# Performance work log

Hardware: AMD Instinct MI355X
Metric: run time of the kernel (lower is better)

The kernel has to match this reference:

```python
import jax, jax.numpy as jnp
import numpy as np

B, N, D = 8, 1024, 512
H, F = 8, 2048
Dh = D // H
EPS = 1e-5
NEG = -1.0e9


def _layernorm(x, g, b):
    mu = jnp.mean(x, axis=-1, keepdims=True)
    var = jnp.mean(jnp.square(x - mu), axis=-1, keepdims=True)
    return (x - mu) * jax.lax.rsqrt(var + EPS) * g + b


def setup_inputs() -> dict:
    key = jax.random.key(0)
    ks = jax.random.split(key, 8)
    s = 0.02  # weight init scale
    return {
        "x": jax.random.normal(ks[0], (B, N, D), jnp.float32),
        "adjacency_logits": jax.random.normal(ks[1], (N, N), jnp.float32),
        "candidate_edge_mask": jax.random.randint(ks[2], (N, N), 0, 2).astype(jnp.bool_),
        "Wq": jax.random.normal(ks[3], (D, D), jnp.float32) * s,
        "Wk": jax.random.normal(ks[4], (D, D), jnp.float32) * s,
        "Wv": jax.random.normal(ks[5], (D, D), jnp.float32) * s,
        "Wo": jax.random.normal(ks[6], (D, D), jnp.float32) * s,
        "W1": jax.random.normal(jax.random.fold_in(key, 10), (F, D), jnp.float32) * s,
        "b1": jnp.zeros((F,), jnp.float32),
        "W2": jax.random.normal(jax.random.fold_in(key, 11), (D, F), jnp.float32) * s,
        "b2": jnp.zeros((D,), jnp.float32),
        "g_ln1": jnp.ones((D,), jnp.float32),
        "beta_ln1": jnp.zeros((D,), jnp.float32),
        "g_ln2": jnp.ones((D,), jnp.float32),
        "beta_ln2": jnp.zeros((D,), jnp.float32),
    }


def reference(x, adjacency_logits, candidate_edge_mask, Wq, Wk, Wv, Wo,
              W1, b1, W2, b2, g_ln1, beta_ln1, g_ln2, beta_ln2):
    b, n, d = x.shape
    # projections: torch Linear is x @ W^T  -> [B,H,N,Dh]
    def proj(W):
        return jnp.einsum('bnd,ed->bne', x, W).reshape(b, n, H, Dh).transpose(0, 2, 1, 3)
    q, k, v = proj(Wq), proj(Wk), proj(Wv)
    scale = 1.0 / jnp.sqrt(jnp.float32(Dh))
    scores = jnp.einsum('bhqd,bhkd->bhqk', q, k) * scale
    scores = scores + adjacency_logits[None, None]
    mask = candidate_edge_mask[None, None]  # [1,1,N,N]
    scores = jnp.where(mask, scores, NEG)
    attn = jax.nn.softmax(scores, axis=-1)
    attn = jnp.where(mask, attn, 0.0)
    ctx = jnp.einsum('bhqk,bhkd->bhqd', attn, v)
    ctx = ctx.transpose(0, 2, 1, 3).reshape(b, n, d)
    attn_out = jnp.einsum('bnd,ed->bne', ctx, Wo)
    z = _layernorm(x + attn_out, g_ln1, beta_ln1)
    h = jax.nn.relu(jnp.einsum('bnd,fd->bnf', z, W1) + b1)
    z_ffn = jnp.einsum('bnf,df->bnd', h, W2) + b2
    out = _layernorm(z + z_ffn, g_ln2, beta_ln2)
    return out, attn.mean(axis=1)
```

## Files before the change

kernel.cpp:

```cpp
#include <hip/hip_runtime.h>
#include <math.h>
#include <stdint.h>


using bf16_t = __bf16;
typedef __attribute__((__ext_vector_type__(8))) __bf16 bf16x8;
typedef __attribute__((__ext_vector_type__(4))) __bf16 bf16x4;
typedef __attribute__((__ext_vector_type__(4))) float  f32x4;

#define DEVI __device__ __forceinline__

DEVI f32x4 mfma16(bf16x8 a, bf16x8 b, f32x4 c) {
  return __builtin_amdgcn_mfma_f32_16x16x32_bf16(a, b, c, 0, 0, 0);
}

DEVI void gload_lds16(const void* g, void* l) {
  __builtin_amdgcn_global_load_lds(
      (const __attribute__((address_space(1))) uint32_t*)g,
      (__attribute__((address_space(3))) uint32_t*)l, 16, 0, 0);
}

#define EPSC  (1e-5f)
#define QSCALE 0.18033688f

__global__ __launch_bounds__(256) void k_cvtall(const float* __restrict__ x,
                                                const float* __restrict__ wq,
                                                const float* __restrict__ wk,
                                                const float* __restrict__ wv,
                                                const float* __restrict__ wo,
                                                const float* __restrict__ w1,
                                                const float* __restrict__ w2,
                                                bf16_t* __restrict__ ox,
                                                bf16_t* __restrict__ owq,
                                                bf16_t* __restrict__ owk,
                                                bf16_t* __restrict__ owv,
                                                bf16_t* __restrict__ owo,
                                                bf16_t* __restrict__ ow1,
                                                bf16_t* __restrict__ ow2) {
  int blk = blockIdx.x;
  const float* src; bf16_t* dst; int base;
  if (blk < 4096)      { src = x;  dst = ox;  base = blk; }
  else {
    blk -= 4096;
    if      (blk < 256)  { src = wq; dst = owq; base = blk; }
    else if (blk < 512)  { src = wk; dst = owk; base = blk - 256; }
    else if (blk < 768)  { src = wv; dst = owv; base = blk - 512; }
    else if (blk < 1024) { src = wo; dst = owo; base = blk - 768; }
    else if (blk < 2048) { src = w1; dst = ow1; base = blk - 1024; }
    else                 { src = w2; dst = ow2; base = blk - 2048; }
  }
  int i = base * 256 + threadIdx.x;
  float4 v = ((const float4*)src)[i];
  bf16x4 o = { (__bf16)v.x, (__bf16)v.y, (__bf16)v.z, (__bf16)v.w };
  ((bf16x4*)dst)[i] = o;
}

__global__ __launch_bounds__(256) void k_prep(const float* __restrict__ adj,
                                              const int* __restrict__ msk,
                                              bf16_t* __restrict__ eadj) {
  int row  = blockIdx.x * 4 + (threadIdx.x >> 6);
  int lane = threadIdx.x & 63;
  for (int i = 0; i < 16; i++) {
    int c = lane + 64 * i;
    size_t idx = (size_t)row * 1024 + c;
    float a = adj[idx];
    bool valid = (msk[idx] != 0);
    eadj[idx] = valid ? (__bf16)__expf(a) : (__bf16)0.f;
  }
}

template<int EPI, int NSPLIT>
__global__ __launch_bounds__(256) void k_gemm(const bf16_t* __restrict__ A,
                                              const bf16_t* __restrict__ B,
                                              int K, int nbx,
                                              const float* __restrict__ bias,
                                              bf16_t* __restrict__ outb,
                                              float* __restrict__ outf,
                                              int out_ncols) {
  __shared__ bf16_t lA[2][4096];
  __shared__ bf16_t lB[2][4096];
  int bid = blockIdx.x;
  int bps = 64 * nbx;
  int split = bid / bps, r = bid - split * bps;
  int nb = r % nbx, mb = r / nbx;
  int KS = K / NSPLIT;
  const bf16_t* Ab = A + (size_t)split * KS;
  const bf16_t* Bb = B + (size_t)split * KS;
  int tid = threadIdx.x, wid = tid >> 6, lane = tid & 63;
  int l16 = lane & 15, g = lane >> 4;
  int wr = wid >> 1, wc = wid & 1;
  int rowbase = mb * 128, c0 = nb * 128;

  int dA0 = wid * 2048 + lane * 16;
  int rA0 = dA0 >> 6;
  int cbA = ((dA0 >> 4) & 3) ^ (rA0 & 3);
  const bf16_t* Asrc0 = Ab + (size_t)(rowbase + rA0) * K + cbA * 8;
  const bf16_t* Asrc1 = Ab + (size_t)(rowbase + rA0 + 16) * K + cbA * 8;
  const bf16_t* Bsrc0 = Bb + (size_t)(c0 + rA0) * K + cbA * 8;
  const bf16_t* Bsrc1 = Bb + (size_t)(c0 + rA0 + 16) * K + cbA * 8;

  f32x4 acc[4][4];
#pragma unroll
  for (int m = 0; m < 4; m++)
#pragma unroll
    for (int n = 0; n < 4; n++) acc[m][n] = (f32x4){0.f, 0.f, 0.f, 0.f};

  gload_lds16(Asrc0, (char*)&lA[0][0] + wid * 2048);
  gload_lds16(Asrc1, (char*)&lA[0][0] + wid * 2048 + 1024);
  gload_lds16(Bsrc0, (char*)&lB[0][0] + wid * 2048);
  gload_lds16(Bsrc1, (char*)&lB[0][0] + wid * 2048 + 1024);
  __syncthreads();

  for (int k0 = 0; k0 < KS; k0 += 32) {
    int buf = (k0 >> 5) & 1;
    if (k0 + 32 < KS) {
      gload_lds16(Asrc0 + k0 + 32, (char*)&lA[buf ^ 1][0] + wid * 2048);
      gload_lds16(Asrc1 + k0 + 32, (char*)&lA[buf ^ 1][0] + wid * 2048 + 1024);
      gload_lds16(Bsrc0 + k0 + 32, (char*)&lB[buf ^ 1][0] + wid * 2048);
      gload_lds16(Bsrc1 + k0 + 32, (char*)&lB[buf ^ 1][0] + wid * 2048 + 1024);
    }
    const char* cA = (const char*)&lA[buf][0];
    const char* cB = (const char*)&lB[buf][0];
    bf16x8 af[4], bq[4];
#pragma unroll
    for (int m = 0; m < 4; m++) {
      int row = wr * 64 + m * 16 + l16;
      af[m] = *(const bf16x8*)(cA + row * 64 + ((g ^ (row & 3)) << 4));
    }
#pragma unroll
    for (int n = 0; n < 4; n++) {
      int row = wc * 64 + n * 16 + l16;
      bq[n] = *(const bf16x8*)(cB + row * 64 + ((g ^ (row & 3)) << 4));
    }
#pragma unroll
    for (int m = 0; m < 4; m++)
#pragma unroll
      for (int n = 0; n < 4; n++) acc[m][n] = mfma16(af[m], bq[n], acc[m][n]);
    __syncthreads();
  }

  int which = c0 / out_ncols;
  int cloc0 = c0 - which * out_ncols;
  size_t obase = (size_t)which * 8192 * out_ncols +
                 (size_t)split * 8192 * out_ncols * (NSPLIT > 1 ? 1 : 0);
  float osc = (EPI == 0 && which == 0) ? QSCALE : 1.0f;
#pragma unroll
  for (int n = 0; n < 4; n++) {
    int col = cloc0 + wc * 64 + n * 16 + l16;
    float bv = (EPI >= 1 && bias && split == 0) ? bias[col] : 0.f;
#pragma unroll
    for (int m = 0; m < 4; m++)
#pragma unroll
      for (int j = 0; j < 4; j++) {
        int row = rowbase + wr * 64 + m * 16 + g * 4 + j;
        float v = acc[m][n][j] + bv;
        size_t idx = obase + (size_t)row * out_ncols + col;
        if (EPI == 1) outb[idx] = (__bf16)fmaxf(v, 0.f);
        else if (EPI == 0) outb[idx] = (__bf16)(v * osc);
        else outf[idx] = v;
      }
  }
}

__global__ __launch_bounds__(256) void k_resln(const float* __restrict__ gin,
                                               int nsplit,
                                               const float* __restrict__ residf,
                                               const bf16_t* __restrict__ residb,
                                               const float* __restrict__ gam,
                                               const float* __restrict__ bet,
                                               float* __restrict__ outf,
                                               bf16_t* __restrict__ outb) {
  const size_t GS = (size_t)8192 * 512;
  int row = blockIdx.x * 4 + (threadIdx.x >> 6);
  int lane = threadIdx.x & 63;
  const float* gp = gin + (size_t)row * 512;
  float4 a0 = ((const float4*)gp)[lane];
  float4 a1 = ((const float4*)gp)[lane + 64];
  for (int s = 1; s < nsplit; s++) {
    const float* gp2 = gp + s * GS;
    float4 r0 = ((const float4*)gp2)[lane];
    float4 r1 = ((const float4*)gp2)[lane + 64];
    a0.x += r0.x; a0.y += r0.y; a0.z += r0.z; a0.w += r0.w;
    a1.x += r1.x; a1.y += r1.y; a1.z += r1.z; a1.w += r1.w;
  }
  if (residf) {
    const float* rp = residf + (size_t)row * 512;
    float4 r0 = ((const float4*)rp)[lane];
    float4 r1 = ((const float4*)rp)[lane + 64];
    a0.x += r0.x; a0.y += r0.y; a0.z += r0.z; a0.w += r0.w;
    a1.x += r1.x; a1.y += r1.y; a1.z += r1.z; a1.w += r1.w;
  } else {
    const bf16_t* rp = residb + (size_t)row * 512;
    bf16x4 r0 = ((const bf16x4*)rp)[lane];
    bf16x4 r1 = ((const bf16x4*)rp)[lane + 64];
    a0.x += (float)r0[0]; a0.y += (float)r0[1]; a0.z += (float)r0[2]; a0.w += (float)r0[3];
    a1.x += (float)r1[0]; a1.y += (float)r1[1]; a1.z += (float)r1[2]; a1.w += (float)r1[3];
  }
  float s = a0.x + a0.y + a0.z + a0.w + a1.x + a1.y + a1.z + a1.w;
  for (int off = 1; off < 64; off <<= 1) s += __shfl_xor(s, off);
  float mu = s * (1.f / 512.f);
  float sq = (a0.x - mu) * (a0.x - mu) + (a0.y - mu) * (a0.y - mu) +
             (a0.z - mu) * (a0.z - mu) + (a0.w - mu) * (a0.w - mu) +
             (a1.x - mu) * (a1.x - mu) + (a1.y - mu) * (a1.y - mu) +
             (a1.z - mu) * (a1.z - mu) + (a1.w - mu) * (a1.w - mu);
  for (int off = 1; off < 64; off <<= 1) sq += __shfl_xor(sq, off);
  float rs = rsqrtf(sq * (1.f / 512.f) + EPSC);

  float4 g0 = ((const float4*)gam)[lane], g1v = ((const float4*)gam)[lane + 64];
  float4 b0 = ((const float4*)bet)[lane], b1v = ((const float4*)bet)[lane + 64];
  float4 o0, o1;
  o0.x = (a0.x - mu) * rs * g0.x + b0.x;  o0.y = (a0.y - mu) * rs * g0.y + b0.y;
  o0.z = (a0.z - mu) * rs * g0.z + b0.z;  o0.w = (a0.w - mu) * rs * g0.w + b0.w;
  o1.x = (a1.x - mu) * rs * g1v.x + b1v.x; o1.y = (a1.y - mu) * rs * g1v.y + b1v.y;
  o1.z = (a1.z - mu) * rs * g1v.z + b1v.z; o1.w = (a1.w - mu) * rs * g1v.w + b1v.w;
  if (outf) {
    float* op = outf + (size_t)row * 512;
    ((float4*)op)[lane] = o0;
    ((float4*)op)[lane + 64] = o1;
  }
  if (outb) {
    bf16_t* op = outb + (size_t)row * 512;
    bf16x4 q0 = { (__bf16)o0.x, (__bf16)o0.y, (__bf16)o0.z, (__bf16)o0.w };
    bf16x4 q1 = { (__bf16)o1.x, (__bf16)o1.y, (__bf16)o1.z, (__bf16)o1.w };
    ((bf16x4*)op)[lane] = q0;
    ((bf16x4*)op)[lane + 64] = q1;
  }
}

__global__ __launch_bounds__(256) void k_vtrans_knorm(const bf16_t* __restrict__ v,
                                                      bf16_t* __restrict__ vT,
                                                      const bf16_t* __restrict__ kk,
                                                      float* __restrict__ kmax) {
  __shared__ bf16_t t[64 * 66];
  __shared__ float red[4];
  int bid = blockIdx.x;
  int tid = threadIdx.x, wid = tid >> 6, lane = tid & 63;
  if (bid < 1024) {
    int nt = bid & 15, h = (bid >> 4) & 7, b = bid >> 7;
    for (int i = 0; i < 16; i++) {
      int n = wid * 16 + i;
      t[lane * 66 + n] = v[(size_t)(b * 1024 + nt * 64 + n) * 512 + h * 64 + lane];
    }
    __syncthreads();
    for (int i = 0; i < 16; i++) {
      int d = wid * 16 + i;
      vT[(size_t)((b * 8 + h) * 64 + d) * 1024 + nt * 64 + lane] = t[d * 66 + lane];
    }
  } else {
    int bh = bid - 1024;
    int b = bh >> 3, h = bh & 7;
    float mx = 0.f;
    for (int n = tid; n < 1024; n += 256) {
      const bf16_t* kp = kk + (size_t)(b * 1024 + n) * 512 + h * 64;
      float ss = 0.f;
#pragma unroll
      for (int vv = 0; vv < 8; vv++) {
        bf16x8 kv = *(const bf16x8*)(kp + vv * 8);
#pragma unroll
        for (int e = 0; e < 8; e++) { float f = (float)kv[e]; ss += f * f; }
      }
      mx = fmaxf(mx, ss);
    }
    for (int off = 1; off < 64; off <<= 1) mx = fmaxf(mx, __shfl_xor(mx, off));
    if (lane == 0) red[wid] = mx;
    __syncthreads();
    if (tid == 0) kmax[bh] = sqrtf(fmaxf(fmaxf(red[0], red[1]), fmaxf(red[2], red[3])));
  }
}

__global__ __launch_bounds__(512) void k_attn_ctx(const bf16_t* __restrict__ q,
                                                  const bf16_t* __restrict__ kk,
                                                  const bf16_t* __restrict__ vT,
                                                  const bf16_t* __restrict__ eadj,
                                                  const float* __restrict__ kmax,
                                                  bf16_t* __restrict__ ctx,
                                                  float* __restrict__ crl) {
  __shared__ bf16_t ldsK[2][4096];
  __shared__ bf16_t ldsV[2][4096];
  __shared__ bf16_t pt[8][16 * 68];
  int bid = blockIdx.x;
  int qt = bid >> 6, h = bid & 7, b = (bid >> 3) & 7;
  int tid = threadIdx.x, wid = tid >> 6, lane = tid & 63;
  int l16 = lane & 15, g = lane >> 4;
  int qg0 = qt * 128 + wid * 16;
  int kvbase = (b * 8 + h) * 64;

  int d0 = wid * 1024 + lane * 16;
  int row0 = d0 >> 7;
  int cb0 = ((d0 >> 4) & 7) ^ (row0 & 7);
  const bf16_t* ksrc = kk + (size_t)(b * 1024) * 512 + h * 64;
  const bf16_t* vsrc = vT + (size_t)kvbase * 1024;

  auto stage = [&](int buf, int kc0) {
    gload_lds16(ksrc + (size_t)(kc0 + row0) * 512 + cb0 * 8, &ldsK[buf][wid * 512]);
    gload_lds16(vsrc + (size_t)row0 * 1024 + kc0 + cb0 * 8, &ldsV[buf][wid * 512]);
  };

  const bf16_t* qp = q + (size_t)(b * 1024 + qg0 + l16) * 512 + h * 64 + 8 * g;
  bf16x8 aq0 = *(const bf16x8*)qp;
  bf16x8 aq1 = *(const bf16x8*)(qp + 32);

  float kmaxv = kmax[b * 8 + h];
  float ssq = 0.f;
#pragma unroll
  for (int e = 0; e < 8; e++) {
    float f0 = (float)aq0[e], f1 = (float)aq1[e];
    ssq += f0 * f0 + f1 * f1;
  }
  ssq += __shfl_xor(ssq, 16);
  ssq += __shfl_xor(ssq, 32);
  float Cn = sqrtf(ssq) * kmaxv;
  float Cj[4];
#pragma unroll
  for (int j = 0; j < 4; j++) Cj[j] = __shfl(Cn, g * 4 + j);

  f32x4 cacc[4];
#pragma unroll
  for (int d = 0; d < 4; d++) cacc[d] = (f32x4){0.f, 0.f, 0.f, 0.f};
  float ls[4] = {0.f, 0.f, 0.f, 0.f};
  bf16_t* myp = pt[wid];
  int rph = l16 & 7;
  const bf16_t* erow = eadj + (size_t)(qg0 + g * 4) * 1024 + l16;

  bf16_t eaA[4][4], eaB[4][4];
  stage(0, 0);
#pragma unroll
  for (int cg = 0; cg < 4; cg++)
#pragma unroll
    for (int j = 0; j < 4; j++) eaA[cg][j] = erow[(size_t)j * 1024 + cg * 16];
  __syncthreads();

  auto tile = [&](int kt, int buf, bf16_t (&eaC)[4][4], bf16_t (&eaN)[4][4]) {
    int kc0 = kt * 64;
    int ktn = (kt + 1 < 16) ? kt + 1 : 15;
    stage(buf ^ 1, ktn * 64);
#pragma unroll
    for (int cg = 0; cg < 4; cg++)
#pragma unroll
      for (int j = 0; j < 4; j++)
        eaN[cg][j] = erow[(size_t)j * 1024 + ktn * 64 + cg * 16];

    const char* curK = (const char*)ldsK[buf];
    const char* curV = (const char*)ldsV[buf];

#pragma unroll
    for (int cg = 0; cg < 4; cg++) {
      const char* krow = curK + ((cg * 16 + l16) << 7);
      bf16x8 k0 = *(const bf16x8*)(krow + ((g ^ rph) << 4));
      bf16x8 k1 = *(const bf16x8*)(krow + (((g + 4) ^ rph) << 4));
      f32x4 s = (f32x4){0.f, 0.f, 0.f, 0.f};
      __builtin_amdgcn_s_setprio(1);
      s = mfma16(aq0, k0, s);
      s = mfma16(aq1, k1, s);
      __builtin_amdgcn_s_setprio(0);
#pragma unroll
      for (int j = 0; j < 4; j++) {
        float p = (float)eaC[cg][j] * exp2f(s[j] - Cj[j]);
        ls[j] += p;
        myp[(g * 4 + j) * 68 + cg * 16 + l16] = (__bf16)p;
      }
    }
#pragma unroll
    for (int half = 0; half < 2; half++) {
      bf16x8 pa = *(const bf16x8*)(myp + l16 * 68 + half * 32 + 8 * g);
      __builtin_amdgcn_s_setprio(1);
#pragma unroll
      for (int dg = 0; dg < 4; dg++) {
        const char* vrow = curV + ((dg * 16 + l16) << 7);
        bf16x8 vv = *(const bf16x8*)(vrow + (((g + half * 4) ^ rph) << 4));
        cacc[dg] = mfma16(pa, vv, cacc[dg]);
      }
      __builtin_amdgcn_s_setprio(0);
    }
    __syncthreads();
  };

  for (int k2 = 0; k2 < 8; k2++) {
    tile(2 * k2,     0, eaA, eaB);
    tile(2 * k2 + 1, 1, eaB, eaA);
  }

#pragma unroll
  for (int j = 0; j < 4; j++)
    for (int off = 1; off < 16; off <<= 1) ls[j] += __shfl_xor(ls[j], off);
  float rc[4];
#pragma unroll
  for (int j = 0; j < 4; j++) rc[j] = (ls[j] > 0.f) ? (1.f / ls[j]) : 0.f;

#pragma unroll
  for (int dg = 0; dg < 4; dg++)
#pragma unroll
    for (int j = 0; j < 4; j++) {
      int row = qg0 + g * 4 + j;
      ctx[(size_t)(b * 1024 + row) * 512 + h * 64 + dg * 16 + l16] =
          (__bf16)(cacc[dg][j] * rc[j]);
    }
  if (l16 == 0) {
#pragma unroll
    for (int j = 0; j < 4; j++) {
      int li = (b * 8 + h) * 1024 + qg0 + g * 4 + j;
      crl[li] = (ls[j] > 0.f) ? (Cj[j] + __log2f(ls[j])) : 1.0e30f;
    }
  }
}

__global__ __launch_bounds__(256, 4) void k_attn_mean(const bf16_t* __restrict__ q,
                                                      const bf16_t* __restrict__ kk,
                                                      const bf16_t* __restrict__ eadj,
                                                      const float* __restrict__ crl,
                                                      float* __restrict__ mout) {
  __shared__ bf16_t lds[4][2][2048];
  int bid = blockIdx.x;
  int kq = bid & 7, qt = (bid >> 3) & 15, b = bid >> 7;
  int tid = threadIdx.x, wid = tid >> 6, lane = tid & 63;
  int l16 = lane & 15, g = lane >> 4;
  int qg0 = qt * 64 + wid * 16;
  int kbase = kq * 128;
  int rl = lane >> 3;
  int cb = (lane & 7) ^ rl;
  const bf16_t* ksrc = kk + (size_t)(b * 1024 + kbase) * 512;

  auto stage = [&](int t) {
    int h = t >> 2, c = t & 3;
    char* dst = (char*)&lds[wid][t & 1][0];
    const bf16_t* sp = ksrc + (size_t)(c * 32 + rl) * 512 + h * 64 + cb * 8;
#pragma unroll
    for (int i = 0; i < 4; i++)
      gload_lds16(sp + (size_t)i * 8 * 512, dst + i * 1024);
  };

  f32x4 macc[8];
#pragma unroll
  for (int kg = 0; kg < 8; kg++) macc[kg] = (f32x4){0.f, 0.f, 0.f, 0.f};

  stage(0);

  for (int h = 0; h < 8; h++) {
    const bf16_t* qp = q + (size_t)(b * 1024 + qg0 + l16) * 512 + h * 64 + 8 * g;
    bf16x8 aq0 = *(const bf16x8*)qp;
    bf16x8 aq1 = *(const bf16x8*)(qp + 32);
    f32x4 CR = *(const f32x4*)(crl + (b * 8 + h) * 1024 + qg0 + g * 4);
#pragma unroll
    for (int c = 0; c < 4; c++) {
      int t = h * 4 + c;
      __builtin_amdgcn_sched_barrier(0);
      if (t < 31) {
        stage(t + 1);
        __builtin_amdgcn_sched_barrier(0);
        asm volatile("s_waitcnt vmcnt(4)" ::: "memory");
      } else {
        asm volatile("s_waitcnt vmcnt(0)" ::: "memory");
      }
      __builtin_amdgcn_sched_barrier(0);
      const char* cK = (const char*)&lds[wid][t & 1][0];
#pragma unroll
      for (int cg = 0; cg < 2; cg++) {
        const char* krow = cK + ((cg * 16 + l16) << 7);
        bf16x8 k0 = *(const bf16x8*)(krow + ((g ^ (l16 & 7)) << 4));
        bf16x8 k1 = *(const bf16x8*)(krow + (((g + 4) ^ (l16 & 7)) << 4));
        f32x4 s = (f32x4){0.f, 0.f, 0.f, 0.f};
        __builtin_amdgcn_s_setprio(1);
        s = mfma16(aq0, k0, s);
        s = mfma16(aq1, k1, s);
        __builtin_amdgcn_s_setprio(0);
        int kg = c * 2 + cg;
#pragma unroll
        for (int j = 0; j < 4; j++)
          macc[kg][j] += exp2f(s[j] - CR[j]);
      }
    }
  }

#pragma unroll
  for (int kg = 0; kg < 8; kg++)
#pragma unroll
    for (int j = 0; j < 4; j++) {
      size_t off = (size_t)(qg0 + g * 4 + j) * 1024 + kbase + kg * 16 + l16;
      mout[(size_t)b * 1048576 + off] = macc[kg][j] * (float)eadj[off] * 0.125f;
    }
}

extern "C" void kernel_launch(void* const* d_in, const int* in_sizes, int n_in,
                              void* d_out, int out_size, void* d_ws, size_t ws_size,
                              hipStream_t stream) {
  (void)in_sizes; (void)n_in; (void)out_size; (void)ws_size;
  const float* x   = (const float*)d_in[0];
  const float* adj = (const float*)d_in[1];
  const int*   msk = (const int*)d_in[2];
  const float* Wq  = (const float*)d_in[3];
  const float* Wk  = (const float*)d_in[4];
  const float* Wv  = (const float*)d_in[5];
  const float* Wo  = (const float*)d_in[6];
  const float* W1  = (const float*)d_in[7];
  const float* b1  = (const float*)d_in[8];
  const float* W2  = (const float*)d_in[9];
  const float* b2  = (const float*)d_in[10];
  const float* g1  = (const float*)d_in[11];
  const float* be1 = (const float*)d_in[12];
  const float* g2  = (const float*)d_in[13];
  const float* be2 = (const float*)d_in[14];

  float* out  = (float*)d_out;
  float* mout = out + (size_t)8 * 1024 * 512;

  char* ws = (char*)d_ws;
  const size_t MB = 1024 * 1024;
  bf16_t* wqb = (bf16_t*)(ws);
  bf16_t* wkb = (bf16_t*)(ws + 512 * 1024);
  bf16_t* wvb = (bf16_t*)(ws + 1 * MB);
  bf16_t* wob = (bf16_t*)(ws + 3 * MB / 2);
  bf16_t* w1b = (bf16_t*)(ws + 2 * MB);
  bf16_t* w2b = (bf16_t*)(ws + 4 * MB);
  float*  crl  = (float*)(ws + 6 * MB + 256 * 1024);
  float*  kmax = (float*)(ws + 6 * MB + 768 * 1024);
  bf16_t* xb   = (bf16_t*)(ws + 8 * MB);
  bf16_t* ctx  = xb;
  bf16_t* zb   = xb;
  bf16_t* qb   = (bf16_t*)(ws + 16 * MB);
  bf16_t* kb   = (bf16_t*)(ws + 24 * MB);
  bf16_t* vb   = (bf16_t*)(ws + 32 * MB);
  bf16_t* vT   = (bf16_t*)(ws + 40 * MB);
  float*  gout1 = (float*)(ws + 16 * MB);
  bf16_t* hb    = (bf16_t*)(ws + 16 * MB);
  float*  gout2 = (float*)(ws + 44 * MB);
  bf16_t* eadj  = (bf16_t*)(ws + 72 * MB);

  k_cvtall<<<7168, 256, 0, stream>>>(x, Wq, Wk, Wv, Wo, W1, W2,
                                     xb, wqb, wkb, wvb, wob, w1b, w2b);

  k_prep<<<256, 256, 0, stream>>>(adj, msk, eadj);

  k_gemm<0, 1><<<64 * 12, 256, 0, stream>>>(xb, wqb, 512, 12, nullptr, qb, nullptr, 512);
  k_vtrans_knorm<<<1088, 256, 0, stream>>>(vb, vT, kb, kmax);

  k_attn_ctx<<<512, 512, 0, stream>>>(qb, kb, vT, eadj, kmax, ctx, crl);
  k_attn_mean<<<1024, 256, 0, stream>>>(qb, kb, eadj, crl, mout);

  k_gemm<2, 2><<<2 * 64 * 4, 256, 0, stream>>>(ctx, wob, 512, 4, nullptr, nullptr, gout1, 512);
  k_resln<<<2048, 256, 0, stream>>>(gout1, 2, x, nullptr, g1, be1, nullptr, zb);
  k_gemm<1, 1><<<64 * 16, 256, 0, stream>>>(zb, w1b, 512, 16, b1, hb, nullptr, 2048);
  k_gemm<2, 2><<<2 * 64 * 4, 256, 0, stream>>>(hb, w2b, 2048, 4, b2, nullptr, gout2, 512);
  k_resln<<<2048, 256, 0, stream>>>(gout2, 2, nullptr, zb, g2, be2, out, nullptr);
}
```

Baseline: 231.3 us.

## Triple-buffer attention K/V pipeline, permute eadj layout, fold prep into convert

Moves the exp(adjacency)/mask prep into the conversion kernel as extra blocks, dropping one launch. The prep now writes a permuted layout, so each lane reads its four adjacency weights as one bf16x4 vector instead of sixteen scalar loads. The attention-context kernel goes from double to triple buffering of K/V tiles, with explicit vmcnt waits and raw s_barrier replacing __syncthreads. The row max offset is folded into the MFMA accumulator init to save a subtract per element. The cost is more LDS per block, which may lower occupancy, and hand-tuned waitcnt counts that must match the number of loads in flight.

```diff
diff --git a/kernel.cpp b/kernel.cpp
--- a/kernel.cpp
+++ b/kernel.cpp
@@ -30,14 +30,30 @@
                                                 const float* __restrict__ wo,
                                                 const float* __restrict__ w1,
                                                 const float* __restrict__ w2,
+                                                const float* __restrict__ adj,
+                                                const int* __restrict__ msk,
                                                 bf16_t* __restrict__ ox,
                                                 bf16_t* __restrict__ owq,
                                                 bf16_t* __restrict__ owk,
                                                 bf16_t* __restrict__ owv,
                                                 bf16_t* __restrict__ owo,
                                                 bf16_t* __restrict__ ow1,
-                                                bf16_t* __restrict__ ow2) {
+                                                bf16_t* __restrict__ ow2,
+                                                bf16_t* __restrict__ eadjP) {
   int blk = blockIdx.x;
+  if (blk >= 7168) {
+    int row  = (blk - 7168) * 4 + (threadIdx.x >> 6);
+    int lane = threadIdx.x & 63;
+    for (int i = 0; i < 16; i++) {
+      int c = lane + 64 * i;
+      size_t idx = (size_t)row * 1024 + c;
+      float a = adj[idx];
+      bool valid = (msk[idx] != 0);
+      int pos = (c & ~63) + ((c & 15) << 2) + ((c >> 4) & 3);
+      eadjP[(size_t)row * 1024 + pos] = valid ? (__bf16)__expf(a) : (__bf16)0.f;
+    }
+    return;
+  }
   const float* src; bf16_t* dst; int base;
   if (blk < 4096)      { src = x;  dst = ox;  base = blk; }
   else {
@@ -53,20 +69,6 @@
   float4 v = ((const float4*)src)[i];
   bf16x4 o = { (__bf16)v.x, (__bf16)v.y, (__bf16)v.z, (__bf16)v.w };
   ((bf16x4*)dst)[i] = o;
-}
-
-__global__ __launch_bounds__(256) void k_prep(const float* __restrict__ adj,
-                                              const int* __restrict__ msk,
-                                              bf16_t* __restrict__ eadj) {
-  int row  = blockIdx.x * 4 + (threadIdx.x >> 6);
-  int lane = threadIdx.x & 63;
-  for (int i = 0; i < 16; i++) {
-    int c = lane + 64 * i;
-    size_t idx = (size_t)row * 1024 + c;
-    float a = adj[idx];
-    bool valid = (msk[idx] != 0);
-    eadj[idx] = valid ? (__bf16)__expf(a) : (__bf16)0.f;
-  }
 }
 
 template<int EPI, int NSPLIT>
@@ -271,12 +273,12 @@
 __global__ __launch_bounds__(512) void k_attn_ctx(const bf16_t* __restrict__ q,
                                                   const bf16_t* __restrict__ kk,
                                                   const bf16_t* __restrict__ vT,
-                                                  const bf16_t* __restrict__ eadj,
+                                                  const bf16_t* __restrict__ eadjP,
                                                   const float* __restrict__ kmax,
                                                   bf16_t* __restrict__ ctx,
                                                   float* __restrict__ crl) {
-  __shared__ bf16_t ldsK[2][4096];
-  __shared__ bf16_t ldsV[2][4096];
+  __shared__ bf16_t ldsK[3][4096];
+  __shared__ bf16_t ldsV[3][4096];
   __shared__ bf16_t pt[8][16 * 68];
   int bid = blockIdx.x;
   int qt = bid >> 6, h = bid & 7, b = (bid >> 3) & 7;
@@ -310,9 +312,9 @@
   ssq += __shfl_xor(ssq, 16);
   ssq += __shfl_xor(ssq, 32);
   float Cn = sqrtf(ssq) * kmaxv;
-  float Cj[4];
-#pragma unroll
-  for (int j = 0; j < 4; j++) Cj[j] = __shfl(Cn, g * 4 + j);
+  f32x4 negC;
+#pragma unroll
+  for (int j = 0; j < 4; j++) negC[j] = -__shfl(Cn, g * 4 + j);
 
   f32x4 cacc[4];
 #pragma unroll
@@ -320,42 +322,30 @@
   float ls[4] = {0.f, 0.f, 0.f, 0.f};
   bf16_t* myp = pt[wid];
   int rph = l16 & 7;
-  const bf16_t* erow = eadj + (size_t)(qg0 + g * 4) * 1024 + l16;
-
-  bf16_t eaA[4][4], eaB[4][4];
-  stage(0, 0);
-#pragma unroll
-  for (int cg = 0; cg < 4; cg++)
-#pragma unroll
-    for (int j = 0; j < 4; j++) eaA[cg][j] = erow[(size_t)j * 1024 + cg * 16];
-  __syncthreads();
-
-  auto tile = [&](int kt, int buf, bf16_t (&eaC)[4][4], bf16_t (&eaN)[4][4]) {
-    int kc0 = kt * 64;
-    int ktn = (kt + 1 < 16) ? kt + 1 : 15;
-    stage(buf ^ 1, ktn * 64);
-#pragma unroll
-    for (int cg = 0; cg < 4; cg++)
-#pragma unroll
-      for (int j = 0; j < 4; j++)
-        eaN[cg][j] = erow[(size_t)j * 1024 + ktn * 64 + cg * 16];
-
+  const bf16_t* erowP = eadjP + (size_t)(qg0 + g * 4) * 1024 + l16 * 4;
+
+  bf16x4 ea0[4], ea1[4];
+  auto loadEA = [&](bf16x4 (&d)[4], int kc0) {
+#pragma unroll
+    for (int j = 0; j < 4; j++)
+      d[j] = *(const bf16x4*)(erowP + (size_t)j * 1024 + kc0);
+  };
+
+  auto computeTile = [&](int buf, const bf16x4 (&eaC)[4]) {
     const char* curK = (const char*)ldsK[buf];
     const char* curV = (const char*)ldsV[buf];
-
 #pragma unroll
     for (int cg = 0; cg < 4; cg++) {
       const char* krow = curK + ((cg * 16 + l16) << 7);
       bf16x8 k0 = *(const bf16x8*)(krow + ((g ^ rph) << 4));
       bf16x8 k1 = *(const bf16x8*)(krow + (((g + 4) ^ rph) << 4));
-      f32x4 s = (f32x4){0.f, 0.f, 0.f, 0.f};
       __builtin_amdgcn_s_setprio(1);
-      s = mfma16(aq0, k0, s);
+      f32x4 s = mfma16(aq0, k0, negC);
       s = mfma16(aq1, k1, s);
       __builtin_amdgcn_s_setprio(0);
 #pragma unroll
       for (int j = 0; j < 4; j++) {
-        float p = (float)eaC[cg][j] * exp2f(s[j] - Cj[j]);
+        float p = (float)eaC[j][cg] * exp2f(s[j]);
         ls[j] += p;
         myp[(g * 4 + j) * 68 + cg * 16 + l16] = (__bf16)p;
       }
@@ -372,12 +362,37 @@
       }
       __builtin_amdgcn_s_setprio(0);
     }
-    __syncthreads();
   };
 
-  for (int k2 = 0; k2 < 8; k2++) {
-    tile(2 * k2,     0, eaA, eaB);
-    tile(2 * k2 + 1, 1, eaB, eaA);
+  stage(0, 0);
+  stage(1, 64);
+  loadEA(ea0, 0);
+  __builtin_amdgcn_sched_barrier(0);
+  asm volatile("s_waitcnt vmcnt(6) lgkmcnt(0)" ::: "memory");
+  __builtin_amdgcn_sched_barrier(0);
+  __builtin_amdgcn_s_barrier();
+  __builtin_amdgcn_sched_barrier(0);
+
+#pragma unroll
+  for (int kt = 0; kt < 16; ++kt) {
+    const int buf = kt % 3;
+    if (kt + 2 < 16) stage((kt + 2) % 3, (kt + 2) * 64);
+    if (kt + 1 < 16) {
+      if ((kt & 1) == 0) loadEA(ea1, (kt + 1) * 64);
+      else               loadEA(ea0, (kt + 1) * 64);
+    }
+    if ((kt & 1) == 0) computeTile(buf, ea0);
+    else               computeTile(buf, ea1);
+    if (kt < 15) {
+      __builtin_amdgcn_sched_barrier(0);
+      if (kt < 14)
+        asm volatile("s_waitcnt vmcnt(6) lgkmcnt(0)" ::: "memory");
+      else
+        asm volatile("s_waitcnt vmcnt(4) lgkmcnt(0)" ::: "memory");
+      __builtin_amdgcn_sched_barrier(0);
+      __builtin_amdgcn_s_barrier();
+      __builtin_amdgcn_sched_barrier(0);
+    }
   }
 
 #pragma unroll
@@ -399,14 +414,14 @@
 #pragma unroll
     for (int j = 0; j < 4; j++) {
       int li = (b * 8 + h) * 1024 + qg0 + g * 4 + j;
-      crl[li] = (ls[j] > 0.f) ? (Cj[j] + __log2f(ls[j])) : 1.0e30f;
+      crl[li] = (ls[j] > 0.f) ? (-negC[j] + __log2f(ls[j])) : 1.0e30f;
     }
   }
 }
 
 __global__ __launch_bounds__(256, 4) void k_attn_mean(const bf16_t* __restrict__ q,
                                                       const bf16_t* __restrict__ kk,
-                                                      const bf16_t* __restrict__ eadj,
+                                                      const bf16_t* __restrict__ eadjP,
                                                       const float* __restrict__ crl,
                                                       float* __restrict__ mout) {
   __shared__ bf16_t lds[4][2][2048];
@@ -440,6 +455,7 @@
     bf16x8 aq0 = *(const bf16x8*)qp;
     bf16x8 aq1 = *(const bf16x8*)(qp + 32);
     f32x4 CR = *(const f32x4*)(crl + (b * 8 + h) * 1024 + qg0 + g * 4);
+    f32x4 negCR = (f32x4){-CR[0], -CR[1], -CR[2], -CR[3]};
 #pragma unroll
     for (int c = 0; c < 4; c++) {
       int t = h * 4 + c;
@@ -458,15 +474,14 @@
         const char* krow = cK + ((cg * 16 + l16) << 7);
         bf16x8 k0 = *(const bf16x8*)(krow + ((g ^ (l16 & 7)) << 4));
         bf16x8 k1 = *(const bf16x8*)(krow + (((g + 4) ^ (l16 & 7)) << 4));
-        f32x4 s = (f32x4){0.f, 0.f, 0.f, 0.f};
         __builtin_amdgcn_s_setprio(1);
-        s = mfma16(aq0, k0, s);
+        f32x4 s = mfma16(aq0, k0, negCR);
         s = mfma16(aq1, k1, s);
         __builtin_amdgcn_s_setprio(0);
         int kg = c * 2 + cg;
 #pragma unroll
         for (int j = 0; j < 4; j++)
-          macc[kg][j] += exp2f(s[j] - CR[j]);
+          macc[kg][j] += exp2f(s[j]);
       }
     }
   }
@@ -475,8 +490,10 @@
   for (int kg = 0; kg < 8; kg++)
 #pragma unroll
     for (int j = 0; j < 4; j++) {
-      size_t off = (size_t)(qg0 + g * 4 + j) * 1024 + kbase + kg * 16 + l16;
-      mout[(size_t)b * 1048576 + off] = macc[kg][j] * (float)eadj[off] * 0.125f;
+      size_t row = qg0 + g * 4 + j;
+      size_t off = row * 1024 + kbase + kg * 16 + l16;
+      size_t poff = row * 1024 + 64 * (kq * 2 + (kg >> 2)) + l16 * 4 + (kg & 3);
+      mout[(size_t)b * 1048576 + off] = macc[kg][j] * (float)eadjP[poff] * 0.125f;
     }
 }
 
@@ -523,18 +540,16 @@
   float*  gout1 = (float*)(ws + 16 * MB);
   bf16_t* hb    = (bf16_t*)(ws + 16 * MB);
   float*  gout2 = (float*)(ws + 44 * MB);
-  bf16_t* eadj  = (bf16_t*)(ws + 72 * MB);
-
-  k_cvtall<<<7168, 256, 0, stream>>>(x, Wq, Wk, Wv, Wo, W1, W2,
-                                     xb, wqb, wkb, wvb, wob, w1b, w2b);
-
-  k_prep<<<256, 256, 0, stream>>>(adj, msk, eadj);
+  bf16_t* eadjP = (bf16_t*)(ws + 72 * MB);
+
+  k_cvtall<<<7424, 256, 0, stream>>>(x, Wq, Wk, Wv, Wo, W1, W2, adj, msk,
+                                     xb, wqb, wkb, wvb, wob, w1b, w2b, eadjP);
 
   k_gemm<0, 1><<<64 * 12, 256, 0, stream>>>(xb, wqb, 512, 12, nullptr, qb, nullptr, 512);
   k_vtrans_knorm<<<1088, 256, 0, stream>>>(vb, vT, kb, kmax);
 
-  k_attn_ctx<<<512, 512, 0, stream>>>(qb, kb, vT, eadj, kmax, ctx, crl);
-  k_attn_mean<<<1024, 256, 0, stream>>>(qb, kb, eadj, crl, mout);
+  k_attn_ctx<<<512, 512, 0, stream>>>(qb, kb, vT, eadjP, kmax, ctx, crl);
+  k_attn_mean<<<1024, 256, 0, stream>>>(qb, kb, eadjP, crl, mout);
 
   k_gemm<2, 2><<<2 * 64 * 4, 256, 0, stream>>>(ctx, wob, 512, 4, nullptr, nullptr, gout1, 512);
   k_resln<<<2048, 256, 0, stream>>>(gout1, 2, x, nullptr, g1, be1, nullptr, zb);
```

Result: slower. 240.6 us (+4.0%).
